# Kernel optimization log

Hardware: AMD Instinct MI355X
Metric: run time of the kernel (lower is better)

The kernel has to match this reference:

```python
import jax, jax.numpy as jnp
import numpy as np

D_MODEL = 512
NHEAD = 8
NUM_LAYERS = 2
INPUT_DIM = 16
DELTA_SCALE = 1.5
LN_EPS = 1e-5


def setup_inputs() -> dict:
    key = jax.random.key(0)
    ks = jax.random.split(key, 16)
    B, S = 16, 1024
    D = D_MODEL
    s_in = 1.0 / np.sqrt(INPUT_DIM)
    s_d = 1.0 / np.sqrt(D)
    return {
        "features": jax.random.normal(ks[0], (B, S, INPUT_DIM), dtype=jnp.float32),
        "hist_w": jax.random.uniform(ks[1], (D, INPUT_DIM), jnp.float32, -s_in, s_in),
        "hist_b": jax.random.uniform(ks[2], (D,), jnp.float32, -s_in, s_in),
        "query_w": jax.random.uniform(ks[3], (D, INPUT_DIM), jnp.float32, -s_in, s_in),
        "query_b": jax.random.uniform(ks[4], (D,), jnp.float32, -s_in, s_in),
        "in_proj_w": jax.random.uniform(ks[5], (NUM_LAYERS, 3 * D, D), jnp.float32, -s_d, s_d),
        "in_proj_b": jnp.zeros((NUM_LAYERS, 3 * D), jnp.float32),
        "attn_out_w": jax.random.uniform(ks[6], (NUM_LAYERS, D, D), jnp.float32, -s_d, s_d),
        "attn_out_b": jnp.zeros((NUM_LAYERS, D), jnp.float32),
        "ln_g": jnp.ones((NUM_LAYERS, D), jnp.float32),
        "ln_b": jnp.zeros((NUM_LAYERS, D), jnp.float32),
        "out_proj_w": jax.random.uniform(ks[7], (1, D), jnp.float32, -s_d, s_d),
        "out_proj_b": jax.random.uniform(ks[8], (1,), jnp.float32, -s_d, s_d),
    }


def _layer_norm(x, g, b):
    mu = jnp.mean(x, axis=-1, keepdims=True)
    var = jnp.var(x, axis=-1, keepdims=True)
    return (x - mu) * jax.lax.rsqrt(var + LN_EPS) * g + b


def _causal_mha(x, kv, wi, bi, wo, bo):
    # x: [B,S,D] queries, kv: [B,S,D] keys/values; query t attends to kv[:t+1]
    B, S, D = x.shape
    hd = D // NHEAD
    wq, wk, wv = wi[:D], wi[D:2 * D], wi[2 * D:]
    bq, bk, bv = bi[:D], bi[D:2 * D], bi[2 * D:]
    q = (x @ wq.T + bq).reshape(B, S, NHEAD, hd)
    k = (kv @ wk.T + bk).reshape(B, S, NHEAD, hd)
    v = (kv @ wv.T + bv).reshape(B, S, NHEAD, hd)
    scale = 1.0 / np.sqrt(hd)
    scores = jnp.einsum('bqhd,bkhd->bhqk', q, k) * scale
    causal = jnp.tril(jnp.ones((S, S), dtype=bool))
    scores = jnp.where(causal, scores, jnp.finfo(scores.dtype).min)
    attn = jax.nn.softmax(scores, axis=-1)
    out = jnp.einsum('bhqk,bkhd->bqhd', attn, v).reshape(B, S, D)
    return out @ wo.T + bo


def reference(features, hist_w, hist_b, query_w, query_b, in_proj_w, in_proj_b,
              attn_out_w, attn_out_b, ln_g, ln_b, out_proj_w, out_proj_b):
    history = features @ hist_w.T + hist_b          # [B,S,D] (fixed K/V)
    x = features @ query_w.T + query_b              # [B,S,D] queries
    for l in range(NUM_LAYERS):
        a = _causal_mha(x, history, in_proj_w[l], in_proj_b[l], attn_out_w[l], attn_out_b[l])
        x = _layer_norm(x + a, ln_g[l], ln_b[l])
    raw = (x @ out_proj_w.T + out_proj_b)[..., 0]   # [B,S]
    return DELTA_SCALE * jnp.tanh(raw)
```

## Files before the change

kernel.cpp:

```cpp
#include <hip/hip_runtime.h>
#include <math.h>

#define DM 512
#define NH 8
#define HD 64
#define BB 16
#define SS 1024
#define NROWS (BB*SS)
#define IND 16
#define KD 512

typedef unsigned short u16;
typedef __attribute__((ext_vector_type(8))) short bf16x8;
typedef __attribute__((ext_vector_type(4))) float f32x4;

static __device__ __forceinline__ u16 f2bf(float f) {
  union { float f; unsigned int u; } v; v.f = f;
  unsigned int r = v.u + 0x7FFFu + ((v.u >> 16) & 1u);
  return (u16)(r >> 16);
}

static __device__ __forceinline__ float dot4(float4 a, float4 b) {
  return a.x*b.x + a.y*b.y + a.z*b.z + a.w*b.w;
}

#define GLOAD_LDS16(gp, lp)                                                  \
  __builtin_amdgcn_global_load_lds(                                          \
      (const __attribute__((address_space(1))) void*)(gp),                   \
      (__attribute__((address_space(3))) void*)(lp), 16, 0, 0)

__global__ __launch_bounds__(256) void k_f2bf_v(const float* __restrict__ in,
                                                u16* __restrict__ out, int n4) {
  int i = blockIdx.x * 256 + threadIdx.x;
  if (i < n4) {
    float4 v = ((const float4*)in)[i];
    ushort4 p;
    p.x = f2bf(v.x); p.y = f2bf(v.y); p.z = f2bf(v.z); p.w = f2bf(v.w);
    ((ushort4*)out)[i] = p;
  }
}

__global__ __launch_bounds__(256) void k_input_proj(
    const float* __restrict__ feat, const float* __restrict__ hw, const float* __restrict__ hb,
    const float* __restrict__ qw, const float* __restrict__ qb,
    u16* __restrict__ histb, float* __restrict__ x, u16* __restrict__ xb) {
  int r0 = blockIdx.x * 16;
  int tid = threadIdx.x;
  int w = tid >> 6, lane = tid & 63;
  __shared__ float f[16][16];
  f[tid >> 4][tid & 15] = feat[(size_t)(r0 + (tid >> 4))*IND + (tid & 15)];
  __syncthreads();

  #pragma unroll
  for (int ch = 0; ch < 2; ch++) {
    int c0 = ch*256 + lane*4;
    {
      float4 wv[4][4];
      #pragma unroll
      for (int j=0;j<4;j++)
        #pragma unroll
        for (int kq=0;kq<4;kq++)
          wv[j][kq] = *(const float4*)(hw + (size_t)(c0+j)*IND + kq*4);
      float b0 = hb[c0], b1 = hb[c0+1], b2 = hb[c0+2], b3 = hb[c0+3];
      #pragma unroll
      for (int rr=0; rr<4; rr++) {
        int row = r0 + w*4 + rr;
        const float4* fr = (const float4*)f[w*4 + rr];
        float4 f0 = fr[0], f1 = fr[1], f2 = fr[2], f3 = fr[3];
        float v0 = b0 + dot4(wv[0][0],f0) + dot4(wv[0][1],f1) + dot4(wv[0][2],f2) + dot4(wv[0][3],f3);
        float v1 = b1 + dot4(wv[1][0],f0) + dot4(wv[1][1],f1) + dot4(wv[1][2],f2) + dot4(wv[1][3],f3);
        float v2 = b2 + dot4(wv[2][0],f0) + dot4(wv[2][1],f1) + dot4(wv[2][2],f2) + dot4(wv[2][3],f3);
        float v3 = b3 + dot4(wv[3][0],f0) + dot4(wv[3][1],f1) + dot4(wv[3][2],f2) + dot4(wv[3][3],f3);
        ushort4 hp; hp.x = f2bf(v0); hp.y = f2bf(v1); hp.z = f2bf(v2); hp.w = f2bf(v3);
        *(ushort4*)&histb[(size_t)row*DM + c0] = hp;
      }
    }
    {
      float4 wv[4][4];
      #pragma unroll
      for (int j=0;j<4;j++)
        #pragma unroll
        for (int kq=0;kq<4;kq++)
          wv[j][kq] = *(const float4*)(qw + (size_t)(c0+j)*IND + kq*4);
      float b0 = qb[c0], b1 = qb[c0+1], b2 = qb[c0+2], b3 = qb[c0+3];
      #pragma unroll
      for (int rr=0; rr<4; rr++) {
        int row = r0 + w*4 + rr;
        const float4* fr = (const float4*)f[w*4 + rr];
        float4 f0 = fr[0], f1 = fr[1], f2 = fr[2], f3 = fr[3];
        float v0 = b0 + dot4(wv[0][0],f0) + dot4(wv[0][1],f1) + dot4(wv[0][2],f2) + dot4(wv[0][3],f3);
        float v1 = b1 + dot4(wv[1][0],f0) + dot4(wv[1][1],f1) + dot4(wv[1][2],f2) + dot4(wv[1][3],f3);
        float v2 = b2 + dot4(wv[2][0],f0) + dot4(wv[2][1],f1) + dot4(wv[2][2],f2) + dot4(wv[2][3],f3);
        float v3 = b3 + dot4(wv[3][0],f0) + dot4(wv[3][1],f1) + dot4(wv[3][2],f2) + dot4(wv[3][3],f3);
        float4 xv; xv.x = v0; xv.y = v1; xv.z = v2; xv.w = v3;
        *(float4*)&x[(size_t)row*DM + c0] = xv;
        ushort4 xp; xp.x = f2bf(v0); xp.y = f2bf(v1); xp.z = f2bf(v2); xp.w = f2bf(v3);
        *(ushort4*)&xb[(size_t)row*DM + c0] = xp;
      }
    }
  }
}

template<int EPI>
__global__ __launch_bounds__(256) void k_bgemm(
    const u16* __restrict__ A, const u16* __restrict__ Wb,
    const float* __restrict__ bias,
    float* __restrict__ Cf, u16* __restrict__ C0h, u16* __restrict__ C1h) {
  __shared__ u16 As[2][128*64];
  __shared__ u16 Bs[2][128*64];
  int bm = blockIdx.y * 128, bn = blockIdx.x * 128;
  int tid = threadIdx.x;
  int wv = tid >> 6, lane = tid & 63;
  int wm = (wv >> 1) * 64, wn = (wv & 1) * 64;
  int lq = lane & 15, g = lane >> 4, l7 = lq & 7;

  int rsub = lane >> 3;
  int sug  = (lane & 7) ^ rsub;
  const u16* Ag = A  + (size_t)(bm + wv*32 + rsub)*KD + sug*8;
  const u16* Bg = Wb + (size_t)(bn + wv*32 + rsub)*KD + sug*8;

  f32x4 acc[4][4];
  #pragma unroll
  for (int mf=0;mf<4;mf++)
    #pragma unroll
    for (int nf=0;nf<4;nf++) acc[mf][nf] = (f32x4){0.f,0.f,0.f,0.f};

  #pragma unroll
  for (int j=0;j<4;j++) {
    GLOAD_LDS16(Ag + (size_t)j*8*KD, &As[0][(wv*32 + j*8)*64]);
    GLOAD_LDS16(Bg + (size_t)j*8*KD, &Bs[0][(wv*32 + j*8)*64]);
  }
  __syncthreads();

  #pragma unroll 1
  for (int t = 0; t < 8; t++) {
    int cur = t & 1;
    if (t < 7) {
      int nxt = cur ^ 1;
      int k0n = (t+1)*64;
      #pragma unroll
      for (int j=0;j<4;j++) {
        GLOAD_LDS16(Ag + (size_t)j*8*KD + k0n, &As[nxt][(wv*32 + j*8)*64]);
        GLOAD_LDS16(Bg + (size_t)j*8*KD + k0n, &Bs[nxt][(wv*32 + j*8)*64]);
      }
    }
    const u16* Ac = As[cur];
    const u16* Bc = Bs[cur];
    #pragma unroll
    for (int ks=0; ks<2; ks++) {
      int un = ((g + 4*ks) ^ l7) << 3;
      bf16x8 af[4], bfr[4];
      #pragma unroll
      for (int mf=0;mf<4;mf++) af[mf]  = *(const bf16x8*)&Ac[(wm + mf*16 + lq)*64 + un];
      #pragma unroll
      for (int nf=0;nf<4;nf++) bfr[nf] = *(const bf16x8*)&Bc[(wn + nf*16 + lq)*64 + un];
      #pragma unroll
      for (int mf=0;mf<4;mf++)
        #pragma unroll
        for (int nf=0;nf<4;nf++)
          acc[mf][nf] = __builtin_amdgcn_mfma_f32_16x16x32_bf16(af[mf], bfr[nf], acc[mf][nf], 0, 0, 0);
    }
    __syncthreads();
  }

  float fb[4];
  #pragma unroll
  for (int nf=0;nf<4;nf++) fb[nf] = bias[bn + wn + nf*16 + lq];
  int m0 = bm + wm + g*4;
  int n0 = bn + wn + lq;

  if (EPI == 1 || (EPI == 2 && bn < 512)) {
    const float sc = (EPI == 1) ? 0.125f : 1.0f;
    #pragma unroll
    for (int mf=0;mf<4;mf++) {
      int mb = m0 + mf*16;
      int b = mb >> 10, s = mb & 1023;
      #pragma unroll
      for (int nf=0;nf<4;nf++) {
        int n = n0 + nf*16;
        int h = (n >> 6) & 7, d = n & 63;
        u16* dst = C0h + (((size_t)(b*NH + h))*SS + s)*HD + d;
        #pragma unroll
        for (int r=0;r<4;r++) dst[r*HD] = f2bf((acc[mf][nf][r] + fb[nf]) * sc);
      }
    }
  } else if (EPI == 2) {
    #pragma unroll
    for (int mf=0;mf<4;mf++) {
      int mb = m0 + mf*16;
      int b = mb >> 10, s = mb & 1023;
      #pragma unroll
      for (int nf=0;nf<4;nf++) {
        int n = n0 + nf*16 - 512;
        int h = n >> 6, d = n & 63;
        ushort4 pk;
        pk.x = f2bf(acc[mf][nf][0] + fb[nf]);
        pk.y = f2bf(acc[mf][nf][1] + fb[nf]);
        pk.z = f2bf(acc[mf][nf][2] + fb[nf]);
        pk.w = f2bf(acc[mf][nf][3] + fb[nf]);
        *(ushort4*)&C1h[(((size_t)(b*NH + h))*HD + d)*SS + s] = pk;
      }
    }
  } else {
    #pragma unroll
    for (int mf=0;mf<4;mf++) {
      #pragma unroll
      for (int r=0;r<4;r++) {
        int m = m0 + mf*16 + r;
        #pragma unroll
        for (int nf=0;nf<4;nf++) {
          int n = n0 + nf*16;
          Cf[(size_t)m*DM + n] = acc[mf][nf][r] + fb[nf] + Cf[(size_t)m*DM + n];
        }
      }
    }
  }
}

__global__ __launch_bounds__(512) void k_attn_mfma(
    const u16* __restrict__ Q, const u16* __restrict__ K,
    const u16* __restrict__ Vt, u16* __restrict__ ctxb) {
  int ip = blockIdx.x;
  int bh = blockIdx.y;
  int b = bh >> 3, h = bh & 7;
  int tid = threadIdx.x;
  int w = tid >> 6, lane = tid & 63;
  int lq = lane & 15, g = lane >> 4;
  int l7 = lq & 7;

  __shared__ u16 Ks[4096];
  __shared__ u16 Vs[4096];
  __shared__ u16 Ps[8192];

  int sr = tid >> 3, su = tid & 7;
  int kw = sr*64 + ((su ^ (sr&7)) << 3);
  const u16* kgb = K + ((size_t)bh*SS + sr)*HD + su*8;
  const u16* vgb = Vt + ((size_t)bh*HD + sr)*SS + su*8;
  int pbase = w*1024;

  bf16x8 kreg = *(const bf16x8*)kgb;
  bf16x8 vreg = *(const bf16x8*)vgb;

  #pragma unroll 1
  for (int half = 0; half < 2; half++) {
    int qt2 = half ? (7 - ip) : ip;
    int last = 2*qt2 + 1;

    const u16* qbase = Q + ((size_t)bh*SS + qt2*128 + w*16 + lq)*HD;
    bf16x8 qa0 = *(const bf16x8*)(qbase + g*8);
    bf16x8 qa1 = *(const bf16x8*)(qbase + g*8 + 32);

    f32x4 o[4];
    #pragma unroll
    for (int nb=0;nb<4;nb++) o[nb] = (f32x4){0.f,0.f,0.f,0.f};
    float mrun[4], lrun[4];
    #pragma unroll
    for (int r=0;r<4;r++) { mrun[r] = -1e30f; lrun[r] = 0.f; }

    #pragma unroll 1
    for (int kt = 0; kt <= last; kt++) {
      __syncthreads();
      *(bf16x8*)&Ks[kw] = kreg;
      *(bf16x8*)&Vs[kw] = vreg;
      __syncthreads();
      if (kt < last) {
        kreg = *(const bf16x8*)(kgb + (size_t)(kt+1)*64*HD);
        vreg = *(const bf16x8*)(vgb + (kt+1)*64);
      } else if (half == 0) {
        kreg = *(const bf16x8*)kgb;
        vreg = *(const bf16x8*)vgb;
      }
      if (kt*64 > qt2*128 + w*16 + 15) continue;

      f32x4 s[4];
      #pragma unroll
      for (int nb=0;nb<4;nb++) s[nb] = (f32x4){0.f,0.f,0.f,0.f};
      #pragma unroll
      for (int ks=0; ks<2; ks++) {
        bf16x8 aq = ks ? qa1 : qa0;
        #pragma unroll
        for (int nb=0;nb<4;nb++) {
          bf16x8 kb = *(const bf16x8*)&Ks[(lq + 16*nb)*64 + (((g + 4*ks) ^ l7) << 3)];
          s[nb] = __builtin_amdgcn_mfma_f32_16x16x32_bf16(aq, kb, s[nb], 0, 0, 0);
        }
      }

      bool diag = (kt*64 + 63 > qt2*128 + w*16);
      #pragma unroll
      for (int r=0;r<4;r++) {
        int qrow = qt2*128 + w*16 + g*4 + r;
        if (diag) {
          #pragma unroll
          for (int nb=0;nb<4;nb++)
            if (kt*64 + lq + 16*nb > qrow) s[nb][r] = -1e30f;
        }
        float rm = fmaxf(fmaxf(s[0][r], s[1][r]), fmaxf(s[2][r], s[3][r]));
        #pragma unroll
        for (int off=1; off<16; off<<=1) rm = fmaxf(rm, __shfl_xor(rm, off));
        float mnew = fmaxf(mrun[r], rm);
        float corr = __expf(mrun[r] - mnew);
        float psum = 0.f;
        int mrow = g*4 + r;
        #pragma unroll
        for (int nb=0;nb<4;nb++) {
          float p = __expf(s[nb][r] - mnew);
          psum += p;
          Ps[pbase + mrow*64 + ((((lq>>3) + 2*nb) ^ (mrow&7)) << 3) + l7] = f2bf(p);
        }
        #pragma unroll
        for (int off=1; off<16; off<<=1) psum += __shfl_xor(psum, off);
        lrun[r] = lrun[r]*corr + psum;
        mrun[r] = mnew;
        #pragma unroll
        for (int nb=0;nb<4;nb++) o[nb][r] *= corr;
      }

      #pragma unroll
      for (int ks=0; ks<2; ks++) {
        bf16x8 pa = *(const bf16x8*)&Ps[pbase + lq*64 + (((g + 4*ks) ^ l7) << 3)];
        #pragma unroll
        for (int nb=0;nb<4;nb++) {
          bf16x8 vb = *(const bf16x8*)&Vs[(lq + 16*nb)*64 + (((g + 4*ks) ^ l7) << 3)];
          o[nb] = __builtin_amdgcn_mfma_f32_16x16x32_bf16(pa, vb, o[nb], 0, 0, 0);
        }
      }
    }

    #pragma unroll
    for (int r=0;r<4;r++) {
      float inv = 1.f / lrun[r];
      int qrow = qt2*128 + w*16 + g*4 + r;
      u16* cp = ctxb + ((size_t)b*SS + qrow)*DM + h*HD;
      #pragma unroll
      for (int nb=0;nb<4;nb++) cp[lq + 16*nb] = f2bf(o[nb][r] * inv);
    }
  }
}

__global__ __launch_bounds__(256) void k_ln(
    float* __restrict__ x, const float* __restrict__ g,
    const float* __restrict__ b, u16* __restrict__ xb) {
  int row = blockIdx.x*4 + (threadIdx.x>>6);
  int lane = threadIdx.x & 63;
  float* xr = x + (size_t)row*DM;
  float vals[8]; float s1=0.f, s2=0.f;
  #pragma unroll
  for (int u=0;u<8;u++){ float vv = xr[lane + 64*u]; vals[u]=vv; s1+=vv; s2+=vv*vv; }
  #pragma unroll
  for (int off=1; off<64; off<<=1){ s1 += __shfl_xor(s1,off); s2 += __shfl_xor(s2,off); }
  float mu  = s1 * (1.0f/DM);
  float var = s2 * (1.0f/DM) - mu*mu;
  float inv = rsqrtf(var + 1e-5f);
  u16* xbr = xb + (size_t)row*DM;
  #pragma unroll
  for (int u=0;u<8;u++){
    int c = lane+64*u;
    float vv = (vals[u]-mu)*inv*g[c] + b[c];
    xr[c] = vv;
    xbr[c] = f2bf(vv);
  }
}

__global__ __launch_bounds__(256) void k_head(
    const float* __restrict__ x, const float* __restrict__ w,
    const float* __restrict__ b, float* __restrict__ out) {
  int row = blockIdx.x*4 + (threadIdx.x>>6);
  int lane = threadIdx.x & 63;
  const float* xr = x + (size_t)row*DM;
  float acc = 0.f;
  #pragma unroll
  for (int u=0;u<8;u++) acc += xr[lane+64*u]*w[lane+64*u];
  #pragma unroll
  for (int off=1; off<64; off<<=1) acc += __shfl_xor(acc,off);
  if (lane == 0) out[row] = 1.5f * tanhf(acc + b[0]);
}

extern "C" void kernel_launch(void* const* d_in, const int* in_sizes, int n_in,
                              void* d_out, int out_size, void* d_ws, size_t ws_size,
                              hipStream_t stream) {
  (void)in_sizes; (void)n_in; (void)out_size; (void)ws_size;
  const float* feat      = (const float*)d_in[0];
  const float* hist_w    = (const float*)d_in[1];
  const float* hist_b    = (const float*)d_in[2];
  const float* query_w   = (const float*)d_in[3];
  const float* query_b   = (const float*)d_in[4];
  const float* in_proj_w = (const float*)d_in[5];
  const float* in_proj_b = (const float*)d_in[6];
  const float* attn_w    = (const float*)d_in[7];
  const float* attn_b    = (const float*)d_in[8];
  const float* ln_g      = (const float*)d_in[9];
  const float* ln_b      = (const float*)d_in[10];
  const float* out_w     = (const float*)d_in[11];
  const float* out_b     = (const float*)d_in[12];
  float* out = (float*)d_out;

  float* ws = (float*)d_ws;
  const size_t P = (size_t)NROWS * DM;
  float* x    = ws;
  u16* xb     = (u16*)(ws + P);
  u16* histb  = xb + P;
  u16* ctxb   = histb + P;
  u16* qbf    = ctxb + P;
  u16* kbf    = qbf + P;
  u16* vtb    = kbf + P;
  u16* wipb   = vtb + P;
  u16* wob    = wipb + (size_t)2*3*DM*DM;

  {
    int n4i = 2*3*DM*DM/4, n4o = 2*DM*DM/4;
    k_f2bf_v<<<(n4i+255)/256, 256, 0, stream>>>(in_proj_w, wipb, n4i);
    k_f2bf_v<<<(n4o+255)/256, 256, 0, stream>>>(attn_w, wob, n4o);
  }
  k_input_proj<<<NROWS/16, 256, 0, stream>>>(feat, hist_w, hist_b, query_w, query_b, histb, x, xb);

  for (int l = 0; l < 2; l++) {
    const u16* wq  = wipb + (size_t)l*3*DM*DM;
    const u16* wkv = wq + (size_t)DM*DM;
    const float* bq  = in_proj_b + (size_t)l*3*DM;
    const float* bkv = bq + DM;
    k_bgemm<1><<<dim3(4, 128), 256, 0, stream>>>(xb,    wq,  bq,  nullptr, qbf, nullptr);
    k_bgemm<2><<<dim3(8, 128), 256, 0, stream>>>(histb, wkv, bkv, nullptr, kbf, vtb);
    dim3 ga(4, BB*NH);
    k_attn_mfma<<<ga, 512, 0, stream>>>(qbf, kbf, vtb, ctxb);
    const u16* wo = wob + (size_t)l*DM*DM;
    const float* bo = attn_b + (size_t)l*DM;
    k_bgemm<3><<<dim3(4, 128), 256, 0, stream>>>(ctxb, wo, bo, x, nullptr, nullptr);
    k_ln<<<NROWS/4, 256, 0, stream>>>(x, ln_g + (size_t)l*DM, ln_b + (size_t)l*DM, xb);
  }
  k_head<<<NROWS/4, 256, 0, stream>>>(x, out_w, out_b, out);
}
```

Before: 412.7 us.

## Merge Q and KV GEMMs into one launch, single-buffer LDS, remap blocks

The separate Q and KV projection GEMM launches are merged into one 1536-block kernel that picks its operands per tile, and the output projection gets its own kernel. Both now use single-buffered LDS tiles with a sync after each load, dropping the double-buffered prefetch to halve shared memory and allow more resident blocks. Block IDs are remapped so blocks spread across the 8 XCDs land on the same M rows, to improve L2 reuse. The cost is that global loads no longer overlap MFMA within a block and must be hidden by occupancy instead.

```diff
diff --git a/kernel.cpp b/kernel.cpp
--- a/kernel.cpp
+++ b/kernel.cpp
@@ -101,14 +101,23 @@
   }
 }
 
-template<int EPI>
-__global__ __launch_bounds__(256) void k_bgemm(
-    const u16* __restrict__ A, const u16* __restrict__ Wb,
-    const float* __restrict__ bias,
-    float* __restrict__ Cf, u16* __restrict__ C0h, u16* __restrict__ C1h) {
-  __shared__ u16 As[2][128*64];
-  __shared__ u16 Bs[2][128*64];
-  int bm = blockIdx.y * 128, bn = blockIdx.x * 128;
+__global__ __launch_bounds__(256) void k_bgemm_qkv(
+    const u16* __restrict__ xb, const u16* __restrict__ histb,
+    const u16* __restrict__ wq, const u16* __restrict__ wkv,
+    const float* __restrict__ bq, const float* __restrict__ bkv,
+    u16* __restrict__ qbf, u16* __restrict__ kbf, u16* __restrict__ vtb) {
+  __shared__ u16 As[128*64];
+  __shared__ u16 Bs[128*64];
+  int bid = blockIdx.x;
+  int wid = (bid & 7)*192 + (bid >> 3);
+  int gx = wid % 12, gy = wid / 12;
+  int bm = gy * 128;
+  bool isQ = gx < 4;
+  int bn = isQ ? gx*128 : (gx-4)*128;
+  const u16* A   = isQ ? xb : histb;
+  const u16* Wbp = (isQ ? wq : wkv) + (size_t)bn*KD;
+  const float* bias = (isQ ? bq : bkv) + bn;
+
   int tid = threadIdx.x;
   int wv = tid >> 6, lane = tid & 63;
   int wm = (wv >> 1) * 64, wn = (wv & 1) * 64;
@@ -116,44 +125,32 @@
 
   int rsub = lane >> 3;
   int sug  = (lane & 7) ^ rsub;
-  const u16* Ag = A  + (size_t)(bm + wv*32 + rsub)*KD + sug*8;
-  const u16* Bg = Wb + (size_t)(bn + wv*32 + rsub)*KD + sug*8;
+  const u16* Ag = A   + (size_t)(bm + wv*32 + rsub)*KD + sug*8;
+  const u16* Bg = Wbp + (size_t)(wv*32 + rsub)*KD + sug*8;
 
   f32x4 acc[4][4];
   #pragma unroll
   for (int mf=0;mf<4;mf++)
     #pragma unroll
     for (int nf=0;nf<4;nf++) acc[mf][nf] = (f32x4){0.f,0.f,0.f,0.f};
-
-  #pragma unroll
-  for (int j=0;j<4;j++) {
-    GLOAD_LDS16(Ag + (size_t)j*8*KD, &As[0][(wv*32 + j*8)*64]);
-    GLOAD_LDS16(Bg + (size_t)j*8*KD, &Bs[0][(wv*32 + j*8)*64]);
-  }
-  __syncthreads();
 
   #pragma unroll 1
   for (int t = 0; t < 8; t++) {
-    int cur = t & 1;
-    if (t < 7) {
-      int nxt = cur ^ 1;
-      int k0n = (t+1)*64;
-      #pragma unroll
-      for (int j=0;j<4;j++) {
-        GLOAD_LDS16(Ag + (size_t)j*8*KD + k0n, &As[nxt][(wv*32 + j*8)*64]);
-        GLOAD_LDS16(Bg + (size_t)j*8*KD + k0n, &Bs[nxt][(wv*32 + j*8)*64]);
-      }
-    }
-    const u16* Ac = As[cur];
-    const u16* Bc = Bs[cur];
+    int k0 = t*64;
+    #pragma unroll
+    for (int j=0;j<4;j++) {
+      GLOAD_LDS16(Ag + (size_t)j*8*KD + k0, &As[(wv*32 + j*8)*64]);
+      GLOAD_LDS16(Bg + (size_t)j*8*KD + k0, &Bs[(wv*32 + j*8)*64]);
+    }
+    __syncthreads();
     #pragma unroll
     for (int ks=0; ks<2; ks++) {
       int un = ((g + 4*ks) ^ l7) << 3;
       bf16x8 af[4], bfr[4];
       #pragma unroll
-      for (int mf=0;mf<4;mf++) af[mf]  = *(const bf16x8*)&Ac[(wm + mf*16 + lq)*64 + un];
-      #pragma unroll
-      for (int nf=0;nf<4;nf++) bfr[nf] = *(const bf16x8*)&Bc[(wn + nf*16 + lq)*64 + un];
+      for (int mf=0;mf<4;mf++) af[mf]  = *(const bf16x8*)&As[(wm + mf*16 + lq)*64 + un];
+      #pragma unroll
+      for (int nf=0;nf<4;nf++) bfr[nf] = *(const bf16x8*)&Bs[(wn + nf*16 + lq)*64 + un];
       #pragma unroll
       for (int mf=0;mf<4;mf++)
         #pragma unroll
@@ -165,12 +162,13 @@
 
   float fb[4];
   #pragma unroll
-  for (int nf=0;nf<4;nf++) fb[nf] = bias[bn + wn + nf*16 + lq];
+  for (int nf=0;nf<4;nf++) fb[nf] = bias[wn + nf*16 + lq];
   int m0 = bm + wm + g*4;
   int n0 = bn + wn + lq;
 
-  if (EPI == 1 || (EPI == 2 && bn < 512)) {
-    const float sc = (EPI == 1) ? 0.125f : 1.0f;
+  if (isQ || bn < 512) {
+    const float sc = isQ ? 0.125f : 1.0f;
+    u16* dstb = isQ ? qbf : kbf;
     #pragma unroll
     for (int mf=0;mf<4;mf++) {
       int mb = m0 + mf*16;
@@ -179,12 +177,12 @@
       for (int nf=0;nf<4;nf++) {
         int n = n0 + nf*16;
         int h = (n >> 6) & 7, d = n & 63;
-        u16* dst = C0h + (((size_t)(b*NH + h))*SS + s)*HD + d;
+        u16* dst = dstb + (((size_t)(b*NH + h))*SS + s)*HD + d;
         #pragma unroll
         for (int r=0;r<4;r++) dst[r*HD] = f2bf((acc[mf][nf][r] + fb[nf]) * sc);
       }
     }
-  } else if (EPI == 2) {
+  } else {
     #pragma unroll
     for (int mf=0;mf<4;mf++) {
       int mb = m0 + mf*16;
@@ -198,20 +196,78 @@
         pk.y = f2bf(acc[mf][nf][1] + fb[nf]);
         pk.z = f2bf(acc[mf][nf][2] + fb[nf]);
         pk.w = f2bf(acc[mf][nf][3] + fb[nf]);
-        *(ushort4*)&C1h[(((size_t)(b*NH + h))*HD + d)*SS + s] = pk;
-      }
-    }
-  } else {
-    #pragma unroll
-    for (int mf=0;mf<4;mf++) {
-      #pragma unroll
-      for (int r=0;r<4;r++) {
-        int m = m0 + mf*16 + r;
-        #pragma unroll
-        for (int nf=0;nf<4;nf++) {
-          int n = n0 + nf*16;
-          Cf[(size_t)m*DM + n] = acc[mf][nf][r] + fb[nf] + Cf[(size_t)m*DM + n];
-        }
+        *(ushort4*)&vtb[(((size_t)(b*NH + h))*HD + d)*SS + s] = pk;
+      }
+    }
+  }
+}
+
+__global__ __launch_bounds__(256) void k_bgemm_o(
+    const u16* __restrict__ A, const u16* __restrict__ Wb,
+    const float* __restrict__ bias, float* __restrict__ Cf) {
+  __shared__ u16 As[128*64];
+  __shared__ u16 Bs[128*64];
+  int bid = blockIdx.x;
+  int wid = (bid & 7)*64 + (bid >> 3);
+  int gx = wid & 3, gy = wid >> 2;
+  int bm = gy * 128, bn = gx * 128;
+
+  int tid = threadIdx.x;
+  int wv = tid >> 6, lane = tid & 63;
+  int wm = (wv >> 1) * 64, wn = (wv & 1) * 64;
+  int lq = lane & 15, g = lane >> 4, l7 = lq & 7;
+
+  int rsub = lane >> 3;
+  int sug  = (lane & 7) ^ rsub;
+  const u16* Ag = A  + (size_t)(bm + wv*32 + rsub)*KD + sug*8;
+  const u16* Bg = Wb + (size_t)(bn + wv*32 + rsub)*KD + sug*8;
+
+  f32x4 acc[4][4];
+  #pragma unroll
+  for (int mf=0;mf<4;mf++)
+    #pragma unroll
+    for (int nf=0;nf<4;nf++) acc[mf][nf] = (f32x4){0.f,0.f,0.f,0.f};
+
+  #pragma unroll 1
+  for (int t = 0; t < 8; t++) {
+    int k0 = t*64;
+    #pragma unroll
+    for (int j=0;j<4;j++) {
+      GLOAD_LDS16(Ag + (size_t)j*8*KD + k0, &As[(wv*32 + j*8)*64]);
+      GLOAD_LDS16(Bg + (size_t)j*8*KD + k0, &Bs[(wv*32 + j*8)*64]);
+    }
+    __syncthreads();
+    #pragma unroll
+    for (int ks=0; ks<2; ks++) {
+      int un = ((g + 4*ks) ^ l7) << 3;
+      bf16x8 af[4], bfr[4];
+      #pragma unroll
+      for (int mf=0;mf<4;mf++) af[mf]  = *(const bf16x8*)&As[(wm + mf*16 + lq)*64 + un];
+      #pragma unroll
+      for (int nf=0;nf<4;nf++) bfr[nf] = *(const bf16x8*)&Bs[(wn + nf*16 + lq)*64 + un];
+      #pragma unroll
+      for (int mf=0;mf<4;mf++)
+        #pragma unroll
+        for (int nf=0;nf<4;nf++)
+          acc[mf][nf] = __builtin_amdgcn_mfma_f32_16x16x32_bf16(af[mf], bfr[nf], acc[mf][nf], 0, 0, 0);
+    }
+    __syncthreads();
+  }
+
+  float fb[4];
+  #pragma unroll
+  for (int nf=0;nf<4;nf++) fb[nf] = bias[bn + wn + nf*16 + lq];
+  int m0 = bm + wm + g*4;
+  int n0 = bn + wn + lq;
+  #pragma unroll
+  for (int mf=0;mf<4;mf++) {
+    #pragma unroll
+    for (int r=0;r<4;r++) {
+      int m = m0 + mf*16 + r;
+      #pragma unroll
+      for (int nf=0;nf<4;nf++) {
+        int n = n0 + nf*16;
+        Cf[(size_t)m*DM + n] = acc[mf][nf][r] + fb[nf] + Cf[(size_t)m*DM + n];
       }
     }
   }
@@ -418,13 +474,12 @@
     const u16* wkv = wq + (size_t)DM*DM;
     const float* bq  = in_proj_b + (size_t)l*3*DM;
     const float* bkv = bq + DM;
-    k_bgemm<1><<<dim3(4, 128), 256, 0, stream>>>(xb,    wq,  bq,  nullptr, qbf, nullptr);
-    k_bgemm<2><<<dim3(8, 128), 256, 0, stream>>>(histb, wkv, bkv, nullptr, kbf, vtb);
+    k_bgemm_qkv<<<1536, 256, 0, stream>>>(xb, histb, wq, wkv, bq, bkv, qbf, kbf, vtb);
     dim3 ga(4, BB*NH);
     k_attn_mfma<<<ga, 512, 0, stream>>>(qbf, kbf, vtb, ctxb);
     const u16* wo = wob + (size_t)l*DM*DM;
     const float* bo = attn_b + (size_t)l*DM;
-    k_bgemm<3><<<dim3(4, 128), 256, 0, stream>>>(ctxb, wo, bo, x, nullptr, nullptr);
+    k_bgemm_o<<<512, 256, 0, stream>>>(ctxb, wo, bo, x);
     k_ln<<<NROWS/4, 256, 0, stream>>>(x, ln_g + (size_t)l*DM, ln_b + (size_t)l*DM, xb);
   }
   k_head<<<NROWS/4, 256, 0, stream>>>(x, out_w, out_b, out);
```

Measured after the change: 397.5 us. -3.7%, faster.
